# Optimization experiments

Hardware: AMD Instinct MI355X
Metric: run time of the kernel (lower is better)

The kernel has to match this reference:

```python
import jax, jax.numpy as jnp
import numpy as np
import math
from jax import lax


def quick_gelu(v):
    return v * jax.nn.sigmoid(1.702 * v)


def setup_inputs() -> dict:
    key = jax.random.key(0)
    k0, k1, k2, k3 = jax.random.split(key, 4)
    B, N, C, dim = 64, 1024, 768, 8
    x = jax.random.normal(k0, (B, N, C), dtype=jnp.float32)
    # adapter_down: Linear(C -> dim), xavier-ish init
    Wd = jax.random.normal(k1, (C, dim), dtype=jnp.float32) * (1.0 / math.sqrt(C))
    bd = jnp.zeros((dim,), dtype=jnp.float32)
    # adapter_conv: Conv2d(dim, dim, 3, stride=1, pad=1), HWIO layout
    Wc = jax.random.normal(k2, (3, 3, dim, dim), dtype=jnp.float32) * (1.0 / math.sqrt(9 * dim))
    bc = jnp.zeros((dim,), dtype=jnp.float32)
    # adapter_up: Linear(dim -> C); torch inits this to zeros, but use small
    # random values so the output/gradients are non-trivial for testing.
    Wu = jax.random.normal(k3, (dim, C), dtype=jnp.float32) * 0.02
    bu = jnp.zeros((C,), dtype=jnp.float32)
    return {"x": x, "Wd": Wd, "bd": bd, "Wc": Wc, "bc": bc, "Wu": Wu, "bu": bu}


def reference(x, Wd, bd, Wc, bc, Wu, bu):
    B, N, C = x.shape
    H = int(math.isqrt(N))  # N is a static perfect square (patch grid)
    dim = Wd.shape[1]
    # down projection: [B, N, C] -> [B, N, dim]
    x_down = jnp.einsum("bnc,cd->bnd", x, Wd) + bd
    # reshape to NHWC patch grid, activate, 3x3 same-pad conv
    x_patch = quick_gelu(x_down.reshape(B, H, H, dim))
    x_patch = lax.conv_general_dilated(
        x_patch, Wc, window_strides=(1, 1), padding="SAME",
        dimension_numbers=("NHWC", "HWIO", "NHWC")) + bc
    # flatten back, activate (dropout = identity in eval), up projection
    x_down = quick_gelu(x_patch.reshape(B, N, dim))
    x_up = jnp.einsum("bnd,dc->bnc", x_down, Wu) + bu
    return x_up
```

## Files before the change

kernel.cpp:

```cpp
#include <hip/hip_runtime.h>

#define B_  64
#define N_  1024
#define H_  32
#define C_  768
#define D_  8

__device__ __forceinline__ float qgelu(float v) {
    return v / (1.0f + __expf(-1.702f * v));
}

__global__ __launch_bounds__(256, 3) void k_down(
    const float* __restrict__ x, const float* __restrict__ Wd,
    const float* __restrict__ bd, float* __restrict__ t1, int nrows)
{
    __shared__ float sW[D_ * C_];
    for (int i = threadIdx.x; i < D_ * C_; i += 256) {
        int d = i / C_, c = i - d * C_;
        sW[i] = Wd[c * D_ + d];
    }
    __syncthreads();

    const int wid  = threadIdx.x >> 6;
    const int lane = threadIdx.x & 63;

    float4 w[3][D_];
#pragma unroll
    for (int k = 0; k < 3; ++k)
#pragma unroll
        for (int d = 0; d < D_; ++d)
            w[k][d] = *(const float4*)&sW[d * C_ + (lane + k * 64) * 4];

    const int dl = 4 * (lane & 1) + 2 * ((lane >> 1) & 1) + ((lane >> 2) & 1);
    const float bias = bd[dl];

    const int nw = gridDim.x * 4;
    for (int row = blockIdx.x * 4 + wid; row < nrows; row += nw) {
        const float4* xr = (const float4*)(x + (size_t)row * C_);
        float acc[D_];
#pragma unroll
        for (int d = 0; d < D_; ++d) acc[d] = 0.0f;

#pragma unroll
        for (int k = 0; k < 3; ++k) {
            const float4 v = xr[lane + k * 64];
#pragma unroll
            for (int d = 0; d < D_; ++d) {
                acc[d] += v.x * w[k][d].x + v.y * w[k][d].y
                        + v.z * w[k][d].z + v.w * w[k][d].w;
            }
        }

        {
            const bool hi = lane & 1;
#pragma unroll
            for (int j = 0; j < 4; ++j) {
                const float a = acc[j], b = acc[j + 4];
                acc[j]     = hi ? b : a;
                acc[j + 4] = hi ? a : b;
            }
#pragma unroll
            for (int j = 0; j < 4; ++j)
                acc[j] += __shfl_xor(acc[j + 4], 1, 64);
        }
        {
            const bool hi = lane & 2;
#pragma unroll
            for (int j = 0; j < 2; ++j) {
                const float a = acc[j], b = acc[j + 2];
                acc[j]     = hi ? b : a;
                acc[j + 2] = hi ? a : b;
            }
#pragma unroll
            for (int j = 0; j < 2; ++j)
                acc[j] += __shfl_xor(acc[j + 2], 2, 64);
        }
        {
            const bool hi = lane & 4;
            const float a = acc[0], b = acc[1];
            acc[0] = hi ? b : a;
            acc[1] = hi ? a : b;
            acc[0] += __shfl_xor(acc[1], 4, 64);
        }
        acc[0] += __shfl_xor(acc[0], 8, 64);
        acc[0] += __shfl_xor(acc[0], 16, 64);
        acc[0] += __shfl_xor(acc[0], 32, 64);

        if (lane < D_)
            t1[(size_t)row * D_ + dl] = qgelu(acc[0] + bias);
    }
}

__global__ __launch_bounds__(256, 4) void k_conv(
    const float* __restrict__ t1, const float* __restrict__ Wc,
    const float* __restrict__ bc, float* __restrict__ t2)
{
    __shared__ float sIn[10 * H_ * D_];
    __shared__ float sWc[9 * D_ * D_];
    __shared__ float sbc[D_];

    const int img   = blockIdx.x >> 2;
    const int strip = blockIdx.x & 3;
    const int h0    = strip * 8;
    const float* in = t1 + (size_t)img * N_ * D_;

#pragma unroll
    for (int j = 0; j < 10; ++j) {
        const int i  = threadIdx.x + j * 256;
        const int lr = i >> 8;
        const int rem = i & 255;
        const int g  = h0 - 1 + lr;
        sIn[i] = (g >= 0 && g < H_) ? in[(size_t)g * H_ * D_ + rem] : 0.0f;
    }
    for (int i = threadIdx.x; i < 9 * D_ * D_; i += 256) sWc[i] = Wc[i];
    if (threadIdx.x < D_) sbc[threadIdx.x] = bc[threadIdx.x];
    __syncthreads();

    const int lh = threadIdx.x >> 5;
    const int w  = threadIdx.x & 31;
    float acc[D_];
#pragma unroll
    for (int co = 0; co < D_; ++co) acc[co] = sbc[co];

#pragma unroll
    for (int kh = 0; kh < 3; ++kh) {
        const int lrow = lh + kh;
#pragma unroll
        for (int kw = 0; kw < 3; ++kw) {
            const int ww = w + kw - 1;
            if (ww < 0 || ww >= H_) continue;
            const float* ip = &sIn[(lrow * H_ + ww) * D_];
            const float* wp = &sWc[(kh * 3 + kw) * D_ * D_];
#pragma unroll
            for (int ci = 0; ci < D_; ++ci) {
                const float iv = ip[ci];
#pragma unroll
                for (int co = 0; co < D_; ++co)
                    acc[co] += iv * wp[ci * D_ + co];
            }
        }
    }
    float4 o0, o1;
    o0.x = qgelu(acc[0]); o0.y = qgelu(acc[1]);
    o0.z = qgelu(acc[2]); o0.w = qgelu(acc[3]);
    o1.x = qgelu(acc[4]); o1.y = qgelu(acc[5]);
    o1.z = qgelu(acc[6]); o1.w = qgelu(acc[7]);
    float* tp = t2 + ((size_t)img * N_ + (size_t)(h0 + lh) * H_ + w) * D_;
    *(float4*)tp       = o0;
    *(float4*)(tp + 4) = o1;
}

__global__ __launch_bounds__(256, 4) void k_up(
    const float* __restrict__ t2, const float* __restrict__ Wu,
    const float* __restrict__ bu, float* __restrict__ out, int nrows)
{
    __shared__ float sW[D_ * C_];
    __shared__ float sb[C_];
    __shared__ float srow[4 * D_];
    for (int i = threadIdx.x; i < D_ * C_; i += 256) sW[i] = Wu[i];
    for (int i = threadIdx.x; i < C_; i += 256) sb[i] = bu[i];
    __syncthreads();

    for (int base = blockIdx.x * 4; base < nrows; base += gridDim.x * 4) {
        if (threadIdx.x < 4 * D_) {
            const int r = threadIdx.x >> 3, d = threadIdx.x & 7;
            const int row = base + r;
            srow[threadIdx.x] = (row < nrows) ? t2[(size_t)row * D_ + d] : 0.0f;
        }
        __syncthreads();
#pragma unroll
        for (int k = 0; k < 3; ++k) {
            const int task = threadIdx.x + k * 256;
            const int r  = task / 192;
            const int c4 = task - r * 192;
            const int row = base + r;
            if (row < nrows) {
                const float* td = &srow[r * D_];
                float4 o = *(const float4*)&sb[c4 * 4];
#pragma unroll
                for (int d = 0; d < D_; ++d) {
                    const float4 w = *(const float4*)&sW[d * C_ + c4 * 4];
                    const float tv = td[d];
                    o.x += tv * w.x; o.y += tv * w.y;
                    o.z += tv * w.z; o.w += tv * w.w;
                }
                *(float4*)&out[(size_t)row * C_ + (size_t)c4 * 4] = o;
            }
        }
        __syncthreads();
    }
}

extern "C" void kernel_launch(void* const* d_in, const int* in_sizes, int n_in,
                              void* d_out, int out_size, void* d_ws, size_t ws_size,
                              hipStream_t stream) {
    const float* x  = (const float*)d_in[0];
    const float* Wd = (const float*)d_in[1];
    const float* bd = (const float*)d_in[2];
    const float* Wc = (const float*)d_in[3];
    const float* bc = (const float*)d_in[4];
    const float* Wu = (const float*)d_in[5];
    const float* bu = (const float*)d_in[6];
    float* out = (float*)d_out;

    const int nrows = B_ * N_;
    float* t1 = (float*)d_ws;
    float* t2 = t1 + (size_t)nrows * D_;

    k_down<<<768, 256, 0, stream>>>(x, Wd, bd, t1, nrows);
    k_conv<<<B_ * 4, 256, 0, stream>>>(t1, Wc, bc, t2);
    k_up<<<1280, 256, 0, stream>>>(t2, Wu, bu, out, nrows);
}
```

Baseline: 117.1 us.

## Process row pairs in down-proj and register-resident weights in up-proj

k_down now handles two rows per wavefront, issuing both rows' loads up front for more memory-level parallelism, and writes both results from 16 lanes. k_up drops the shared-memory staging and per-iteration __syncthreads. Each wavefront instead keeps its slice of Wu and the bias in registers and produces one output row per iteration, reading the 8-element row straight from global memory. This adds register pressure (96 float4 weights in k_up) and lowers the occupancy hint to 3 blocks, with a smaller grid of 768.

```diff
diff --git a/kernel.cpp b/kernel.cpp
--- a/kernel.cpp
+++ b/kernel.cpp
@@ -8,6 +8,43 @@
 
 __device__ __forceinline__ float qgelu(float v) {
     return v / (1.0f + __expf(-1.702f * v));
+}
+
+__device__ __forceinline__ void reduce8(float* acc, int lane) {
+    {
+        const bool hi = lane & 1;
+#pragma unroll
+        for (int j = 0; j < 4; ++j) {
+            const float a = acc[j], b = acc[j + 4];
+            acc[j] = hi ? b : a;
+            acc[j + 4] = hi ? a : b;
+        }
+#pragma unroll
+        for (int j = 0; j < 4; ++j)
+            acc[j] += __shfl_xor(acc[j + 4], 1, 64);
+    }
+    {
+        const bool hi = lane & 2;
+#pragma unroll
+        for (int j = 0; j < 2; ++j) {
+            const float a = acc[j], b = acc[j + 2];
+            acc[j] = hi ? b : a;
+            acc[j + 2] = hi ? a : b;
+        }
+#pragma unroll
+        for (int j = 0; j < 2; ++j)
+            acc[j] += __shfl_xor(acc[j + 2], 2, 64);
+    }
+    {
+        const bool hi = lane & 4;
+        const float a = acc[0], b = acc[1];
+        acc[0] = hi ? b : a;
+        acc[1] = hi ? a : b;
+        acc[0] += __shfl_xor(acc[1], 4, 64);
+    }
+    acc[0] += __shfl_xor(acc[0], 8, 64);
+    acc[0] += __shfl_xor(acc[0], 16, 64);
+    acc[0] += __shfl_xor(acc[0], 32, 64);
 }
 
 __global__ __launch_bounds__(256, 3) void k_down(
@@ -34,60 +71,43 @@
     const int dl = 4 * (lane & 1) + 2 * ((lane >> 1) & 1) + ((lane >> 2) & 1);
     const float bias = bd[dl];
 
-    const int nw = gridDim.x * 4;
-    for (int row = blockIdx.x * 4 + wid; row < nrows; row += nw) {
-        const float4* xr = (const float4*)(x + (size_t)row * C_);
-        float acc[D_];
-#pragma unroll
-        for (int d = 0; d < D_; ++d) acc[d] = 0.0f;
-
+    const int npairs = nrows >> 1;
+    const int stride = gridDim.x * 4;
+    for (int p = blockIdx.x * 4 + wid; p < npairs; p += stride) {
+        const int r0 = p * 2;
+        const float4* x0 = (const float4*)(x + (size_t)r0 * C_);
+        const float4* x1 = x0 + (C_ / 4);
+
+        float4 v0[3], v1[3];
 #pragma unroll
         for (int k = 0; k < 3; ++k) {
-            const float4 v = xr[lane + k * 64];
+            v0[k] = x0[lane + k * 64];
+            v1[k] = x1[lane + k * 64];
+        }
+
+        float a0[D_], a1[D_];
+#pragma unroll
+        for (int d = 0; d < D_; ++d) { a0[d] = 0.0f; a1[d] = 0.0f; }
+
+#pragma unroll
+        for (int k = 0; k < 3; ++k) {
 #pragma unroll
             for (int d = 0; d < D_; ++d) {
-                acc[d] += v.x * w[k][d].x + v.y * w[k][d].y
-                        + v.z * w[k][d].z + v.w * w[k][d].w;
+                a0[d] += v0[k].x * w[k][d].x + v0[k].y * w[k][d].y
+                       + v0[k].z * w[k][d].z + v0[k].w * w[k][d].w;
+                a1[d] += v1[k].x * w[k][d].x + v1[k].y * w[k][d].y
+                       + v1[k].z * w[k][d].z + v1[k].w * w[k][d].w;
             }
         }
 
-        {
-            const bool hi = lane & 1;
-#pragma unroll
-            for (int j = 0; j < 4; ++j) {
-                const float a = acc[j], b = acc[j + 4];
-                acc[j]     = hi ? b : a;
-                acc[j + 4] = hi ? a : b;
-            }
-#pragma unroll
-            for (int j = 0; j < 4; ++j)
-                acc[j] += __shfl_xor(acc[j + 4], 1, 64);
-        }
-        {
-            const bool hi = lane & 2;
-#pragma unroll
-            for (int j = 0; j < 2; ++j) {
-                const float a = acc[j], b = acc[j + 2];
-                acc[j]     = hi ? b : a;
-                acc[j + 2] = hi ? a : b;
-            }
-#pragma unroll
-            for (int j = 0; j < 2; ++j)
-                acc[j] += __shfl_xor(acc[j + 2], 2, 64);
-        }
-        {
-            const bool hi = lane & 4;
-            const float a = acc[0], b = acc[1];
-            acc[0] = hi ? b : a;
-            acc[1] = hi ? a : b;
-            acc[0] += __shfl_xor(acc[1], 4, 64);
-        }
-        acc[0] += __shfl_xor(acc[0], 8, 64);
-        acc[0] += __shfl_xor(acc[0], 16, 64);
-        acc[0] += __shfl_xor(acc[0], 32, 64);
-
-        if (lane < D_)
-            t1[(size_t)row * D_ + dl] = qgelu(acc[0] + bias);
+        reduce8(a0, lane);
+        reduce8(a1, lane);
+
+        if (lane < 16) {
+            const float s = (lane & 8) ? a1[0] : a0[0];
+            const int   r = r0 + ((lane >> 3) & 1);
+            t1[(size_t)r * D_ + dl] = qgelu(s + bias);
+        }
     }
 }
 
@@ -150,44 +170,42 @@
     *(float4*)(tp + 4) = o1;
 }
 
-__global__ __launch_bounds__(256, 4) void k_up(
+__global__ __launch_bounds__(256, 3) void k_up(
     const float* __restrict__ t2, const float* __restrict__ Wu,
     const float* __restrict__ bu, float* __restrict__ out, int nrows)
 {
-    __shared__ float sW[D_ * C_];
-    __shared__ float sb[C_];
-    __shared__ float srow[4 * D_];
-    for (int i = threadIdx.x; i < D_ * C_; i += 256) sW[i] = Wu[i];
-    for (int i = threadIdx.x; i < C_; i += 256) sb[i] = bu[i];
-    __syncthreads();
-
-    for (int base = blockIdx.x * 4; base < nrows; base += gridDim.x * 4) {
-        if (threadIdx.x < 4 * D_) {
-            const int r = threadIdx.x >> 3, d = threadIdx.x & 7;
-            const int row = base + r;
-            srow[threadIdx.x] = (row < nrows) ? t2[(size_t)row * D_ + d] : 0.0f;
-        }
-        __syncthreads();
-#pragma unroll
-        for (int k = 0; k < 3; ++k) {
-            const int task = threadIdx.x + k * 256;
-            const int r  = task / 192;
-            const int c4 = task - r * 192;
-            const int row = base + r;
-            if (row < nrows) {
-                const float* td = &srow[r * D_];
-                float4 o = *(const float4*)&sb[c4 * 4];
-#pragma unroll
-                for (int d = 0; d < D_; ++d) {
-                    const float4 w = *(const float4*)&sW[d * C_ + c4 * 4];
-                    const float tv = td[d];
-                    o.x += tv * w.x; o.y += tv * w.y;
-                    o.z += tv * w.z; o.w += tv * w.w;
-                }
-                *(float4*)&out[(size_t)row * C_ + (size_t)c4 * 4] = o;
+    const int wid  = threadIdx.x >> 6;
+    const int lane = threadIdx.x & 63;
+
+    float4 w[3][D_];
+    float4 bias[3];
+#pragma unroll
+    for (int j = 0; j < 3; ++j) {
+        bias[j] = *(const float4*)&bu[(lane + j * 64) * 4];
+#pragma unroll
+        for (int d = 0; d < D_; ++d)
+            w[j][d] = *(const float4*)&Wu[d * C_ + (lane + j * 64) * 4];
+    }
+
+    const int stride = gridDim.x * 4;
+    for (int row = blockIdx.x * 4 + wid; row < nrows; row += stride) {
+        const float4* rp = (const float4*)(t2 + (size_t)row * D_);
+        const float4 ra = rp[0];
+        const float4 rb = rp[1];
+        const float rv[D_] = { ra.x, ra.y, ra.z, ra.w, rb.x, rb.y, rb.z, rb.w };
+
+#pragma unroll
+        for (int j = 0; j < 3; ++j) {
+            float4 o = bias[j];
+#pragma unroll
+            for (int d = 0; d < D_; ++d) {
+                o.x += rv[d] * w[j][d].x;
+                o.y += rv[d] * w[j][d].y;
+                o.z += rv[d] * w[j][d].z;
+                o.w += rv[d] * w[j][d].w;
             }
-        }
-        __syncthreads();
+            *(float4*)&out[(size_t)row * C_ + (size_t)(lane + j * 64) * 4] = o;
+        }
     }
 }
 
@@ -209,5 +227,5 @@
 
     k_down<<<768, 256, 0, stream>>>(x, Wd, bd, t1, nrows);
     k_conv<<<B_ * 4, 256, 0, stream>>>(t1, Wc, bc, t2);
-    k_up<<<1280, 256, 0, stream>>>(t2, Wu, bu, out, nrows);
-}
+    k_up<<<768, 256, 0, stream>>>(t2, Wu, bu, out, nrows);
+}
```

Result: no change. 118.5 us (+1.1%).
